# Kernel optimization log

Measured on AMD Instinct MI355X. Metric: run time of the kernel, lower is better.

## Reference

```python
import jax, jax.numpy as jnp
import numpy as np

OUT = 7          # roi_layer out_size
SR = 2           # roi_layer sample_num (sampling ratio)
STRIDES = (4, 8, 16, 32)
FINEST_SCALE = 56.0


def roi_align_level(feat, rois, spatial_scale):
    """RoIAlign (aligned=False, torchvision/mmdet classic) for all rois on one level.
    feat: (B, C, H, W), rois: (K, 5) [batch_idx, x1, y1, x2, y2] in image coords.
    Returns (K, C, OUT, OUT)."""
    B, C, H, W = feat.shape
    b = rois[:, 0].astype(jnp.int32)
    x1 = rois[:, 1] * spatial_scale
    y1 = rois[:, 2] * spatial_scale
    x2 = rois[:, 3] * spatial_scale
    y2 = rois[:, 4] * spatial_scale
    roi_w = jnp.maximum(x2 - x1, 1.0)
    roi_h = jnp.maximum(y2 - y1, 1.0)
    bin_w = roi_w / OUT
    bin_h = roi_h / OUT
    # per-bin sample offsets: (OUT, SR) fractional bin positions
    off = jnp.arange(OUT, dtype=jnp.float32)[:, None] + (jnp.arange(SR, dtype=jnp.float32)[None, :] + 0.5) / SR
    ys = y1[:, None, None] + off[None] * bin_h[:, None, None]   # (K, OUT, SR)
    xs = x1[:, None, None] + off[None] * bin_w[:, None, None]   # (K, OUT, SR)
    y = ys[:, :, :, None, None]                                  # (K, OUT, SR, 1, 1)
    x = xs[:, None, None, :, :]                                  # (K, 1, 1, OUT, SR)
    y, x = jnp.broadcast_arrays(y, x)                            # (K, OUT, SR, OUT, SR)
    valid = (y > -1.0) & (y < H) & (x > -1.0) & (x < W)
    yc = jnp.clip(y, 0.0, H - 1.0)
    xc = jnp.clip(x, 0.0, W - 1.0)
    y0 = jnp.floor(yc)
    x0 = jnp.floor(xc)
    ly = yc - y0
    lx = xc - x0
    hy = 1.0 - ly
    hx = 1.0 - lx
    y0i = y0.astype(jnp.int32)
    x0i = x0.astype(jnp.int32)
    y1i = jnp.minimum(y0i + 1, H - 1)
    x1i = jnp.minimum(x0i + 1, W - 1)
    bb = jnp.broadcast_to(b[:, None, None, None, None], y0i.shape)

    def g(yi, xi):
        # advanced indexing (batched gather) -> (K, OUT, SR, OUT, SR, C)
        return feat[bb, :, yi, xi]

    val = (hy * hx)[..., None] * g(y0i, x0i) \
        + (hy * lx)[..., None] * g(y0i, x1i) \
        + (ly * hx)[..., None] * g(y1i, x0i) \
        + (ly * lx)[..., None] * g(y1i, x1i)
    val = jnp.where(valid[..., None], val, 0.0)
    pooled = val.mean(axis=(2, 4))           # average SRxSR samples -> (K, OUT, OUT, C)
    return jnp.transpose(pooled, (0, 3, 1, 2))  # (K, C, OUT, OUT)


def map_roi_levels(rois, num_levels):
    scale = jnp.sqrt((rois[:, 3] - rois[:, 1] + 1.0) * (rois[:, 4] - rois[:, 2] + 1.0))
    lvl = jnp.floor(jnp.log2(scale / FINEST_SCALE + 1e-6))
    return jnp.clip(lvl, 0, num_levels - 1).astype(jnp.int32)


def setup_inputs() -> dict:
    key = jax.random.key(0)
    ks = jax.random.split(key, 10)
    B, C = 2, 256
    IMG_H, IMG_W = 800.0, 1344.0
    feats = {}
    shapes = [(B, C, 200, 336), (B, C, 100, 168), (B, C, 50, 84), (B, C, 25, 42)]
    for i, s in enumerate(shapes):
        feats[f"feat{i}"] = jax.random.normal(ks[i], s, dtype=jnp.float32)
    K = 1024
    bidx = jax.random.randint(ks[4], (K,), 0, B).astype(jnp.float32)
    # log-uniform box sizes in [16, ~724] px so all 4 FPN levels get rois
    w = 2.0 ** jax.random.uniform(ks[5], (K,), minval=4.0, maxval=9.5)
    h = 2.0 ** jax.random.uniform(ks[6], (K,), minval=4.0, maxval=9.5)
    cx = jax.random.uniform(ks[7], (K,), minval=0.0, maxval=IMG_W)
    cy = jax.random.uniform(ks[8], (K,), minval=0.0, maxval=IMG_H)
    x1 = jnp.clip(cx - w * 0.5, 0.0, IMG_W - 2.0)
    y1 = jnp.clip(cy - h * 0.5, 0.0, IMG_H - 2.0)
    x2 = jnp.clip(x1 + w, x1 + 1.0, IMG_W - 1.0)
    y2 = jnp.clip(y1 + h, y1 + 1.0, IMG_H - 1.0)
    rois = jnp.stack([bidx, x1, y1, x2, y2], axis=-1).astype(jnp.float32)
    feats["rois"] = rois
    return feats


def reference(feat0, feat1, feat2, feat3, rois):
    feats = [feat0, feat1, feat2, feat3]
    num_levels = len(feats)
    target_lvls = map_roi_levels(rois, num_levels)
    K = rois.shape[0]
    C = feats[0].shape[1]
    roi_feats = jnp.zeros((K, C, OUT, OUT), dtype=feats[0].dtype)
    for i in range(num_levels):
        ri = roi_align_level(feats[i], rois, 1.0 / STRIDES[i])
        mask = (target_lvls == i)[:, None, None, None]
        roi_feats = roi_feats + jnp.where(mask, ri, 0.0)
    return roi_feats
```

## Files before the change

### kernel.cpp

```cpp
#include <hip/hip_runtime.h>
#include <stdint.h>
#include <stddef.h>

#define C_TOTAL   256
#define CPG       4
#define NGROUPS   (C_TOTAL / CPG)
#define NBINS     49
#define NSAMP     196
#define TILE_D    1280
#define SD_STRIDE 16
#define BLOB_DW   (NSAMP * 8)
#define DESC_CHUNKS (BLOB_DW / 4)
#define WCHUNK    (DESC_CHUNKS / 4)

__global__ __launch_bounds__(256)
void roi_desc_kernel(const float* __restrict__ rois, int* __restrict__ ws_i,
                     int blobBase )
{
    const int k   = blockIdx.x;
    const int tid = threadIdx.x;

    const float bf  = rois[k * 5 + 0];
    const float rx1 = rois[k * 5 + 1];
    const float ry1 = rois[k * 5 + 2];
    const float rx2 = rois[k * 5 + 3];
    const float ry2 = rois[k * 5 + 4];
    const int   b   = (int)bf;

    const float scale = sqrtf((rx2 - rx1 + 1.0f) * (ry2 - ry1 + 1.0f));
    int lvl = (int)floorf(log2f(scale / 56.0f + 1e-6f));
    lvl = lvl < 0 ? 0 : (lvl > 3 ? 3 : lvl);

    int H, W;
    if      (lvl == 0) { H = 200; W = 336; }
    else if (lvl == 1) { H = 100; W = 168; }
    else if (lvl == 2) { H =  50; W =  84; }
    else               { H =  25; W =  42; }

    const float ss  = 1.0f / (float)(4 << lvl);
    const float x1s = rx1 * ss, y1s = ry1 * ss;
    const float x2s = rx2 * ss, y2s = ry2 * ss;
    const float roi_w = fmaxf(x2s - x1s, 1.0f);
    const float roi_h = fmaxf(y2s - y1s, 1.0f);
    const float bw = roi_w * (1.0f / 7.0f);
    const float bh = roi_h * (1.0f / 7.0f);

    const float Hm1 = (float)(H - 1), Wm1 = (float)(W - 1);
    const int ty0 = (int)floorf(fminf(fmaxf(y1s + 0.25f * bh, 0.0f), Hm1));
    const int tx0 = (int)floorf(fminf(fmaxf(x1s + 0.25f * bw, 0.0f), Wm1));
    const int ty1 = min((int)floorf(fminf(fmaxf(y1s + 6.75f * bh, 0.0f), Hm1)) + 1, H - 1);
    const int tx1 = min((int)floorf(fminf(fmaxf(x1s + 6.75f * bw, 0.0f), Wm1)) + 1, W - 1);
    const int fh = ty1 - ty0 + 1;
    const int fw = tx1 - tx0 + 1;

    int cpr = (fw + (tx0 & 3) + 3) >> 2;
    if (cpr > (W >> 2)) cpr = W >> 2;
    const bool use16 = (lvl < 3) && (fh * cpr <= TILE_D / 4);

    int rb, rowStride, chunks;
    if (use16) {
        rb = tx0 & ~3;
        if (rb + 4 * cpr > W) rb = W - 4 * cpr;
        rowStride = 4 * cpr;
        chunks = fh * cpr;
        if (chunks > TILE_D / 4) chunks = TILE_D / 4;
    } else {
        rb = tx0;
        rowStride = fw;
        chunks = fh * fw;
        if (chunks > TILE_D) chunks = TILE_D;
    }
    const uint32_t d = use16 ? (uint32_t)cpr : (uint32_t)fw;
    const uint32_t M = (1u << 22) / d + 1u;
    const int dW = W - rowStride;

    if (tid == 0) {
        int* sd = ws_i + k * SD_STRIDE;
        sd[0] = lvl;
        sd[1] = use16 ? 1 : 0;
        sd[2] = b * C_TOTAL * H * W + ty0 * W + rb;
        sd[3] = chunks;
        sd[4] = (int)M;
        sd[5] = dW;
        sd[6] = H * W;
    }

    if (tid < NSAMP) {
        const int iy = tid / 14;
        const int ix = tid - iy * 14;
        const float yy = y1s + ((float)iy * 0.5f + 0.25f) * bh;
        const float xx = x1s + ((float)ix * 0.5f + 0.25f) * bw;
        const bool valid = (yy > -1.0f) && (yy < (float)H) && (xx > -1.0f) && (xx < (float)W);
        const float yc  = fminf(fmaxf(yy, 0.0f), Hm1);
        const float xc  = fminf(fmaxf(xx, 0.0f), Wm1);
        const float y0f = floorf(yc);
        const float x0f = floorf(xc);
        const float ly = yc - y0f, lx = xc - x0f;
        const float hy = 1.0f - ly, hx = 1.0f - lx;
        const int y0  = (int)y0f, x0 = (int)x0f;
        const int y1i = min(y0 + 1, H - 1);
        const int x1i = min(x0 + 1, W - 1);
        const int r0 = (y0  - ty0) * rowStride - rb;
        const int r1 = (y1i - ty0) * rowStride - rb;
        const float v = valid ? 0.25f : 0.0f;
        float4* w4 = (float4*)(ws_i + blobBase + k * BLOB_DW);
        int4*   c4 = (int4*)  (ws_i + blobBase + k * BLOB_DW + 4 * NSAMP);
        w4[tid] = make_float4(hy * hx * v, hy * lx * v, ly * hx * v, ly * lx * v);
        c4[tid] = make_int4(r0 + x0, r0 + x1i, r1 + x0, r1 + x1i);
    }
}

__global__ __launch_bounds__(256, 6)
void roi_align_main(const float* __restrict__ f0,
                    const float* __restrict__ f1,
                    const float* __restrict__ f2,
                    const float* __restrict__ f3,
                    const int* __restrict__ ws_i,
                    float* __restrict__ out,
                    int blobBase)
{
    __shared__ __align__(16) float s_tile[CPG * TILE_D];
    __shared__ __align__(16) float s_desc[BLOB_DW];

    const int k    = blockIdx.y;
    const int g    = blockIdx.x;
    const int tid  = threadIdx.x;
    const int wv   = tid >> 6;
    const int lane = tid & 63;

    const int* sd = ws_i + k * SD_STRIDE;
    const int lvl     = sd[0];
    const int use16   = sd[1];
    const int srcBase = sd[2];
    const int chunks  = sd[3];
    const uint32_t M  = (uint32_t)sd[4];
    const int dW      = sd[5];
    const int HW      = sd[6];

    const float* feat = (lvl == 0) ? f0 : (lvl == 1) ? f1 : (lvl == 2) ? f2 : f3;

    {
        const int c = g * CPG + wv;
        const float* src = feat + srcBase + (size_t)c * (size_t)HW;
        float* dst = s_tile + wv * TILE_D;
        if (use16) {
            for (int start = 0; start < chunks; start += 64) {
                int s = (start + 64 > chunks) ? max(chunks - 64, 0) : start;
                int idx = s + lane;
                if (idx >= chunks) idx = chunks - 1;
                const int fy  = (int)(((uint32_t)idx * M) >> 22);
                const int off = (idx << 2) + fy * dW;
                __builtin_amdgcn_global_load_lds(
                    (const __attribute__((address_space(1))) uint32_t*)(src + off),
                    (__attribute__((address_space(3))) uint32_t*)(dst + (s << 2)),
                    16, 0, 0);
            }
        } else {
            for (int start = 0; start < chunks; start += 64) {
                int s = (start + 64 > chunks) ? max(chunks - 64, 0) : start;
                int idx = s + lane;
                if (idx >= chunks) idx = chunks - 1;
                const int fy  = (int)(((uint32_t)idx * M) >> 22);
                const int off = idx + fy * dW;
                __builtin_amdgcn_global_load_lds(
                    (const __attribute__((address_space(1))) uint32_t*)(src + off),
                    (__attribute__((address_space(3))) uint32_t*)(dst + s),
                    4, 0, 0);
            }
        }
    }

    {
        const float* bsrc = (const float*)(ws_i + blobBase + k * BLOB_DW);
        const int i0 = wv * WCHUNK;
        __builtin_amdgcn_global_load_lds(
            (const __attribute__((address_space(1))) uint32_t*)(bsrc + ((i0 + lane) << 2)),
            (__attribute__((address_space(3))) uint32_t*)(s_desc + (i0 << 2)),
            16, 0, 0);
        __builtin_amdgcn_global_load_lds(
            (const __attribute__((address_space(1))) uint32_t*)(bsrc + ((i0 + WCHUNK - 64 + lane) << 2)),
            (__attribute__((address_space(3))) uint32_t*)(s_desc + ((i0 + WCHUNK - 64) << 2)),
            16, 0, 0);
    }

    asm volatile("s_waitcnt vmcnt(0)" ::: "memory");
    __syncthreads();

    if (lane < NBINS) {
        const float*  t  = s_tile + wv * TILE_D;
        const float4* w4 = (const float4*)s_desc;
        const int4*   c4 = (const int4*)(s_desc + 4 * NSAMP);
        const int oy = lane / 7;
        const int ox = lane - oy * 7;
        const int sbase = oy * 28 + ox * 2;
        float acc = 0.0f;
#pragma unroll
        for (int sy = 0; sy < 2; ++sy) {
#pragma unroll
            for (int sx = 0; sx < 2; ++sx) {
                const int s = sbase + sy * 14 + sx;
                const float4 w  = w4[s];
                const int4   cc = c4[s];
                acc += w.x * t[cc.x] + w.y * t[cc.y]
                     + w.z * t[cc.z] + w.w * t[cc.w];
            }
        }
        const int c = g * CPG + wv;
        out[((size_t)k * C_TOTAL + c) * NBINS + lane] = acc;
    }
}

extern "C" void kernel_launch(void* const* d_in, const int* in_sizes, int n_in,
                              void* d_out, int out_size, void* d_ws, size_t ws_size,
                              hipStream_t stream) {
    const float* f0   = (const float*)d_in[0];
    const float* f1   = (const float*)d_in[1];
    const float* f2   = (const float*)d_in[2];
    const float* f3   = (const float*)d_in[3];
    const float* rois = (const float*)d_in[4];
    float* out = (float*)d_out;
    int*   ws  = (int*)d_ws;

    const int K = in_sizes[4] / 5;
    const int blobBase = K * SD_STRIDE;

    roi_desc_kernel<<<K, 256, 0, stream>>>(rois, ws, blobBase);

    dim3 grid(NGROUPS, K, 1);
    roi_align_main<<<grid, 256, 0, stream>>>(f0, f1, f2, f3, ws, out, blobBase);
}
```

Baseline: 146.1 us.

## Convert RoIAlign main kernel to persistent chains with double-buffered LDS prefetch

Replaces the one-block-per-(roi, channel-group) grid with a fixed grid of 8 chains per channel group. Each block loops over rois with stride 8 and double-buffers the feature tile and descriptor blob in LDS. The next roi's global-to-LDS loads are issued before computing the current one, and a counted vmcnt wait replaces the full drain. This is meant to hide load latency and cut per-block launch and setup overhead. In exchange, occupancy drops to 2 blocks per CU with twice the LDS per block, and total parallelism is much lower.

```diff
diff --git a/kernel.cpp b/kernel.cpp
--- a/kernel.cpp
+++ b/kernel.cpp
@@ -12,10 +12,11 @@
 #define BLOB_DW   (NSAMP * 8)
 #define DESC_CHUNKS (BLOB_DW / 4)
 #define WCHUNK    (DESC_CHUNKS / 4)
+#define NCHAIN    8
 
 __global__ __launch_bounds__(256)
 void roi_desc_kernel(const float* __restrict__ rois, int* __restrict__ ws_i,
-                     int blobBase )
+                     int blobBase)
 {
     const int k   = blockIdx.x;
     const int tid = threadIdx.x;
@@ -110,103 +111,146 @@
     }
 }
 
-__global__ __launch_bounds__(256, 6)
-void roi_align_main(const float* __restrict__ f0,
-                    const float* __restrict__ f1,
-                    const float* __restrict__ f2,
-                    const float* __restrict__ f3,
-                    const int* __restrict__ ws_i,
-                    float* __restrict__ out,
-                    int blobBase)
+struct SDesc { int lvl, use16, srcBase, chunks, M, dW, HW; };
+
+__device__ __forceinline__ SDesc load_sd(const int* __restrict__ p) {
+    SDesc s;
+    s.lvl = p[0]; s.use16 = p[1]; s.srcBase = p[2]; s.chunks = p[3];
+    s.M = p[4]; s.dW = p[5]; s.HW = p[6];
+    return s;
+}
+
+#define WV_CASE(N) case N: asm volatile("s_waitcnt vmcnt(" #N ")" ::: "memory"); break;
+__device__ __forceinline__ void wait_vm(int n) {
+    switch (n) {
+        WV_CASE(1) WV_CASE(2) WV_CASE(3) WV_CASE(4) WV_CASE(5)
+        WV_CASE(6) WV_CASE(7) WV_CASE(8) WV_CASE(9) WV_CASE(10)
+        WV_CASE(11) WV_CASE(12) WV_CASE(13) WV_CASE(14) WV_CASE(15)
+        WV_CASE(16) WV_CASE(17)
+        default: asm volatile("s_waitcnt vmcnt(0)" ::: "memory"); break;
+    }
+}
+
+__device__ __forceinline__ int stage_issue(float* __restrict__ tbuf, float* __restrict__ dbuf,
+                                           const SDesc& sd, int k, int g, int wv, int lane,
+                                           const float* __restrict__ f0, const float* __restrict__ f1,
+                                           const float* __restrict__ f2, const float* __restrict__ f3,
+                                           const int* __restrict__ ws_i, int blobBase)
 {
-    __shared__ __align__(16) float s_tile[CPG * TILE_D];
-    __shared__ __align__(16) float s_desc[BLOB_DW];
-
-    const int k    = blockIdx.y;
-    const int g    = blockIdx.x;
-    const int tid  = threadIdx.x;
-    const int wv   = tid >> 6;
-    const int lane = tid & 63;
-
-    const int* sd = ws_i + k * SD_STRIDE;
-    const int lvl     = sd[0];
-    const int use16   = sd[1];
-    const int srcBase = sd[2];
-    const int chunks  = sd[3];
-    const uint32_t M  = (uint32_t)sd[4];
-    const int dW      = sd[5];
-    const int HW      = sd[6];
-
-    const float* feat = (lvl == 0) ? f0 : (lvl == 1) ? f1 : (lvl == 2) ? f2 : f3;
-
-    {
-        const int c = g * CPG + wv;
-        const float* src = feat + srcBase + (size_t)c * (size_t)HW;
-        float* dst = s_tile + wv * TILE_D;
-        if (use16) {
-            for (int start = 0; start < chunks; start += 64) {
-                int s = (start + 64 > chunks) ? max(chunks - 64, 0) : start;
-                int idx = s + lane;
-                if (idx >= chunks) idx = chunks - 1;
-                const int fy  = (int)(((uint32_t)idx * M) >> 22);
-                const int off = (idx << 2) + fy * dW;
-                __builtin_amdgcn_global_load_lds(
-                    (const __attribute__((address_space(1))) uint32_t*)(src + off),
-                    (__attribute__((address_space(3))) uint32_t*)(dst + (s << 2)),
-                    16, 0, 0);
+    const float* feat = (sd.lvl == 0) ? f0 : (sd.lvl == 1) ? f1 : (sd.lvl == 2) ? f2 : f3;
+    const int c = g * CPG + wv;
+    const float* src = feat + sd.srcBase + (size_t)c * (size_t)sd.HW;
+    float* dst = tbuf + wv * TILE_D;
+    const uint32_t M = (uint32_t)sd.M;
+    const int chunks = sd.chunks, dW = sd.dW;
+    int n = 0;
+    if (sd.use16) {
+        for (int start = 0; start < chunks; start += 64) {
+            int s = (start + 64 > chunks) ? max(chunks - 64, 0) : start;
+            int idx = s + lane;
+            if (idx >= chunks) idx = chunks - 1;
+            const int fy  = (int)(((uint32_t)idx * M) >> 22);
+            const int off = (idx << 2) + fy * dW;
+            __builtin_amdgcn_global_load_lds(
+                (const __attribute__((address_space(1))) uint32_t*)(src + off),
+                (__attribute__((address_space(3))) uint32_t*)(dst + (s << 2)),
+                16, 0, 0);
+            ++n;
+        }
+    } else {
+        for (int start = 0; start < chunks; start += 64) {
+            int s = (start + 64 > chunks) ? max(chunks - 64, 0) : start;
+            int idx = s + lane;
+            if (idx >= chunks) idx = chunks - 1;
+            const int fy  = (int)(((uint32_t)idx * M) >> 22);
+            const int off = idx + fy * dW;
+            __builtin_amdgcn_global_load_lds(
+                (const __attribute__((address_space(1))) uint32_t*)(src + off),
+                (__attribute__((address_space(3))) uint32_t*)(dst + s),
+                4, 0, 0);
+            ++n;
+        }
+    }
+    const float* bsrc = (const float*)(ws_i + blobBase + k * BLOB_DW);
+    const int i0 = wv * WCHUNK;
+    __builtin_amdgcn_global_load_lds(
+        (const __attribute__((address_space(1))) uint32_t*)(bsrc + ((i0 + lane) << 2)),
+        (__attribute__((address_space(3))) uint32_t*)(dbuf + (i0 << 2)),
+        16, 0, 0);
+    __builtin_amdgcn_global_load_lds(
+        (const __attribute__((address_space(1))) uint32_t*)(bsrc + ((i0 + WCHUNK - 64 + lane) << 2)),
+        (__attribute__((address_space(3))) uint32_t*)(dbuf + ((i0 + WCHUNK - 64) << 2)),
+        16, 0, 0);
+    return n + 2;
+}
+
+__global__ __launch_bounds__(256, 2)
+void roi_align_chain(const float* __restrict__ f0,
+                     const float* __restrict__ f1,
+                     const float* __restrict__ f2,
+                     const float* __restrict__ f3,
+                     const int* __restrict__ ws_i,
+                     float* __restrict__ out,
+                     int blobBase, int K)
+{
+    __shared__ __align__(16) float s_tile[2][CPG * TILE_D];
+    __shared__ __align__(16) float s_desc[2][BLOB_DW];
+
+    const int g     = blockIdx.x;
+    const int chain = blockIdx.y;
+    const int tid   = threadIdx.x;
+    const int wv    = tid >> 6;
+    const int lane  = tid & 63;
+
+    if (chain >= K) return;
+
+    const int RPC = (K - chain + NCHAIN - 1) / NCHAIN;
+
+    SDesc sd0 = load_sd(ws_i + chain * SD_STRIDE);
+    stage_issue(s_tile[0], s_desc[0], sd0, chain, g, wv, lane, f0, f1, f2, f3, ws_i, blobBase);
+    int k1 = chain + NCHAIN; if (k1 >= K) k1 = K - 1;
+    SDesc sdn = load_sd(ws_i + k1 * SD_STRIDE);
+
+    for (int i = 0; i < RPC; ++i) {
+        const int k   = chain + i * NCHAIN;
+        const int cur = i & 1;
+
+        int nn = 0;
+        if (i + 1 < RPC)
+            nn = stage_issue(s_tile[cur ^ 1], s_desc[cur ^ 1], sdn, k + NCHAIN,
+                             g, wv, lane, f0, f1, f2, f3, ws_i, blobBase);
+
+        int kpre = chain + (i + 2) * NCHAIN;
+        if (kpre >= K) kpre = K - 1;
+        SDesc pre = load_sd(ws_i + kpre * SD_STRIDE);
+
+        wait_vm(nn);
+        __syncthreads();
+
+        if (lane < NBINS) {
+            const float*  t  = s_tile[cur] + wv * TILE_D;
+            const float4* w4 = (const float4*)s_desc[cur];
+            const int4*   c4 = (const int4*)(s_desc[cur] + 4 * NSAMP);
+            const int oy = lane / 7;
+            const int ox = lane - oy * 7;
+            const int sbase = oy * 28 + ox * 2;
+            float acc = 0.0f;
+#pragma unroll
+            for (int sy = 0; sy < 2; ++sy) {
+#pragma unroll
+                for (int sx = 0; sx < 2; ++sx) {
+                    const int s = sbase + sy * 14 + sx;
+                    const float4 w  = w4[s];
+                    const int4   cc = c4[s];
+                    acc += w.x * t[cc.x] + w.y * t[cc.y]
+                         + w.z * t[cc.z] + w.w * t[cc.w];
+                }
             }
-        } else {
-            for (int start = 0; start < chunks; start += 64) {
-                int s = (start + 64 > chunks) ? max(chunks - 64, 0) : start;
-                int idx = s + lane;
-                if (idx >= chunks) idx = chunks - 1;
-                const int fy  = (int)(((uint32_t)idx * M) >> 22);
-                const int off = idx + fy * dW;
-                __builtin_amdgcn_global_load_lds(
-                    (const __attribute__((address_space(1))) uint32_t*)(src + off),
-                    (__attribute__((address_space(3))) uint32_t*)(dst + s),
-                    4, 0, 0);
-            }
+            const int c = g * CPG + wv;
+            out[((size_t)k * C_TOTAL + c) * NBINS + lane] = acc;
         }
-    }
-
-    {
-        const float* bsrc = (const float*)(ws_i + blobBase + k * BLOB_DW);
-        const int i0 = wv * WCHUNK;
-        __builtin_amdgcn_global_load_lds(
-            (const __attribute__((address_space(1))) uint32_t*)(bsrc + ((i0 + lane) << 2)),
-            (__attribute__((address_space(3))) uint32_t*)(s_desc + (i0 << 2)),
-            16, 0, 0);
-        __builtin_amdgcn_global_load_lds(
-            (const __attribute__((address_space(1))) uint32_t*)(bsrc + ((i0 + WCHUNK - 64 + lane) << 2)),
-            (__attribute__((address_space(3))) uint32_t*)(s_desc + ((i0 + WCHUNK - 64) << 2)),
-            16, 0, 0);
-    }
-
-    asm volatile("s_waitcnt vmcnt(0)" ::: "memory");
-    __syncthreads();
-
-    if (lane < NBINS) {
-        const float*  t  = s_tile + wv * TILE_D;
-        const float4* w4 = (const float4*)s_desc;
-        const int4*   c4 = (const int4*)(s_desc + 4 * NSAMP);
-        const int oy = lane / 7;
-        const int ox = lane - oy * 7;
-        const int sbase = oy * 28 + ox * 2;
-        float acc = 0.0f;
-#pragma unroll
-        for (int sy = 0; sy < 2; ++sy) {
-#pragma unroll
-            for (int sx = 0; sx < 2; ++sx) {
-                const int s = sbase + sy * 14 + sx;
-                const float4 w  = w4[s];
-                const int4   cc = c4[s];
-                acc += w.x * t[cc.x] + w.y * t[cc.y]
-                     + w.z * t[cc.z] + w.w * t[cc.w];
-            }
-        }
-        const int c = g * CPG + wv;
-        out[((size_t)k * C_TOTAL + c) * NBINS + lane] = acc;
+        __syncthreads();
+        sdn = pre;
     }
 }
 
@@ -226,6 +270,6 @@
 
     roi_desc_kernel<<<K, 256, 0, stream>>>(rois, ws, blobBase);
 
-    dim3 grid(NGROUPS, K, 1);
-    roi_align_main<<<grid, 256, 0, stream>>>(f0, f1, f2, f3, ws, out, blobBase);
-}
+    dim3 grid(NGROUPS, NCHAIN, 1);
+    roi_align_chain<<<grid, 256, 0, stream>>>(f0, f1, f2, f3, ws, out, blobBase, K);
+}
```

Measured after the change: 197.3 us. +35.0%, slower.

## Sort RoIs by level and Morton-ordered center to improve L2 locality

Applied to the files above, without the earlier changes.

Adds a single-block bitonic sort kernel that orders RoIs by FPN level and a Z-order code of their box center, then launches the main kernel in that sorted order so neighbouring blocks read overlapping feature regions. The main kernel no longer stages the sample descriptor blob through LDS and instead reads weights and indices directly from global memory into registers; the smaller LDS footprint allows the occupancy hint to be raised from 6 to 7. The cost is an extra serial one-block launch plus a permuted descriptor copy. The sort path is only taken when K is at most 1024.

```diff
diff --git a/kernel.cpp b/kernel.cpp
--- a/kernel.cpp
+++ b/kernel.cpp
@@ -10,12 +10,12 @@
 #define TILE_D    1280
 #define SD_STRIDE 16
 #define BLOB_DW   (NSAMP * 8)
-#define DESC_CHUNKS (BLOB_DW / 4)
-#define WCHUNK    (DESC_CHUNKS / 4)
+#define SORTN     1024
+
 
 __global__ __launch_bounds__(256)
 void roi_desc_kernel(const float* __restrict__ rois, int* __restrict__ ws_i,
-                     int blobBase )
+                     int blobBase, int kbase)
 {
     const int k   = blockIdx.x;
     const int tid = threadIdx.x;
@@ -83,6 +83,19 @@
         sd[4] = (int)M;
         sd[5] = dW;
         sd[6] = H * W;
+        sd[7] = k;
+        const float cx = 0.5f * (rx1 + rx2);
+        const float cy = 0.5f * (ry1 + ry2);
+        int qx = (int)(cx * (64.0f / 1344.0f));
+        int qy = (int)(cy * (64.0f / 800.0f));
+        qx = qx < 0 ? 0 : (qx > 63 ? 63 : qx);
+        qy = qy < 0 ? 0 : (qy > 63 ? 63 : qy);
+        unsigned m = 0;
+#pragma unroll
+        for (int j = 0; j < 6; ++j)
+            m |= (((unsigned)(qx >> j) & 1u) << (2 * j)) |
+                 (((unsigned)(qy >> j) & 1u) << (2 * j + 1));
+        ws_i[kbase + k] = (int)(((unsigned)lvl << 22) | (m << 10) | (unsigned)k);
     }
 
     if (tid < NSAMP) {
@@ -103,32 +116,63 @@
         const int r0 = (y0  - ty0) * rowStride - rb;
         const int r1 = (y1i - ty0) * rowStride - rb;
         const float v = valid ? 0.25f : 0.0f;
-        float4* w4 = (float4*)(ws_i + blobBase + k * BLOB_DW);
-        int4*   c4 = (int4*)  (ws_i + blobBase + k * BLOB_DW + 4 * NSAMP);
+        float4* w4 = (float4*)(ws_i + blobBase + (size_t)k * BLOB_DW);
+        int4*   c4 = (int4*)  (ws_i + blobBase + (size_t)k * BLOB_DW + 4 * NSAMP);
         w4[tid] = make_float4(hy * hx * v, hy * lx * v, ly * hx * v, ly * lx * v);
         c4[tid] = make_int4(r0 + x0, r0 + x1i, r1 + x0, r1 + x1i);
     }
 }
 
-__global__ __launch_bounds__(256, 6)
+__global__ __launch_bounds__(256)
+void roi_sort_kernel(int* __restrict__ ws_i, int K, int kbase, int sbase)
+{
+    __shared__ unsigned skey[SORTN];
+    const int tid = threadIdx.x;
+
+    const bool do_sort = (K <= SORTN);
+    if (do_sort) {
+        for (int i = tid; i < SORTN; i += 256)
+            skey[i] = (i < K) ? (unsigned)ws_i[kbase + i] : 0xFFFFFFFFu;
+        __syncthreads();
+        for (unsigned size = 2; size <= SORTN; size <<= 1) {
+            for (unsigned stride = size >> 1; stride; stride >>= 1) {
+                for (int i = tid; i < SORTN; i += 256) {
+                    const unsigned p = (unsigned)i ^ stride;
+                    if (p > (unsigned)i) {
+                        const bool up = ((i & size) == 0);
+                        const unsigned a = skey[i], b = skey[p];
+                        if ((a > b) == up) { skey[i] = b; skey[p] = a; }
+                    }
+                }
+                __syncthreads();
+            }
+        }
+    }
+    for (int i = tid; i < K * SD_STRIDE; i += 256) {
+        const int rank = i >> 4, j = i & 15;
+        const int k = do_sort ? (int)(skey[rank] & 1023u) : rank;
+        ws_i[sbase + i] = ws_i[k * SD_STRIDE + j];
+    }
+}
+
+__global__ __launch_bounds__(256, 7)
 void roi_align_main(const float* __restrict__ f0,
                     const float* __restrict__ f1,
                     const float* __restrict__ f2,
                     const float* __restrict__ f3,
                     const int* __restrict__ ws_i,
                     float* __restrict__ out,
-                    int blobBase)
+                    int blobBase, int sbase)
 {
     __shared__ __align__(16) float s_tile[CPG * TILE_D];
-    __shared__ __align__(16) float s_desc[BLOB_DW];
-
-    const int k    = blockIdx.y;
+
+    const int rank = blockIdx.y;
     const int g    = blockIdx.x;
     const int tid  = threadIdx.x;
     const int wv   = tid >> 6;
     const int lane = tid & 63;
 
-    const int* sd = ws_i + k * SD_STRIDE;
+    const int* sd = ws_i + sbase + rank * SD_STRIDE;
     const int lvl     = sd[0];
     const int use16   = sd[1];
     const int srcBase = sd[2];
@@ -136,6 +180,7 @@
     const uint32_t M  = (uint32_t)sd[4];
     const int dW      = sd[5];
     const int HW      = sd[6];
+    const int k       = sd[7];
 
     const float* feat = (lvl == 0) ? f0 : (lvl == 1) ? f1 : (lvl == 2) ? f2 : f3;
 
@@ -170,40 +215,32 @@
         }
     }
 
-    {
-        const float* bsrc = (const float*)(ws_i + blobBase + k * BLOB_DW);
-        const int i0 = wv * WCHUNK;
-        __builtin_amdgcn_global_load_lds(
-            (const __attribute__((address_space(1))) uint32_t*)(bsrc + ((i0 + lane) << 2)),
-            (__attribute__((address_space(3))) uint32_t*)(s_desc + (i0 << 2)),
-            16, 0, 0);
-        __builtin_amdgcn_global_load_lds(
-            (const __attribute__((address_space(1))) uint32_t*)(bsrc + ((i0 + WCHUNK - 64 + lane) << 2)),
-            (__attribute__((address_space(3))) uint32_t*)(s_desc + ((i0 + WCHUNK - 64) << 2)),
-            16, 0, 0);
-    }
-
     asm volatile("s_waitcnt vmcnt(0)" ::: "memory");
     __syncthreads();
 
     if (lane < NBINS) {
         const float*  t  = s_tile + wv * TILE_D;
-        const float4* w4 = (const float4*)s_desc;
-        const int4*   c4 = (const int4*)(s_desc + 4 * NSAMP);
+        const float4* w4 = (const float4*)(ws_i + blobBase + (size_t)k * BLOB_DW);
+        const int4*   c4 = (const int4*)(ws_i + blobBase + (size_t)k * BLOB_DW + 4 * NSAMP);
         const int oy = lane / 7;
         const int ox = lane - oy * 7;
-        const int sbase = oy * 28 + ox * 2;
+        const int sbin = oy * 28 + ox * 2;
+
+        float4 w[4]; int4 cc[4];
+#pragma unroll
+        for (int sy = 0; sy < 2; ++sy)
+#pragma unroll
+            for (int sx = 0; sx < 2; ++sx) {
+                const int s = sbin + sy * 14 + sx;
+                w[sy * 2 + sx]  = w4[s];
+                cc[sy * 2 + sx] = c4[s];
+            }
+
         float acc = 0.0f;
 #pragma unroll
-        for (int sy = 0; sy < 2; ++sy) {
-#pragma unroll
-            for (int sx = 0; sx < 2; ++sx) {
-                const int s = sbase + sy * 14 + sx;
-                const float4 w  = w4[s];
-                const int4   cc = c4[s];
-                acc += w.x * t[cc.x] + w.y * t[cc.y]
-                     + w.z * t[cc.z] + w.w * t[cc.w];
-            }
+        for (int i = 0; i < 4; ++i) {
+            acc += w[i].x * t[cc[i].x] + w[i].y * t[cc[i].y]
+                 + w[i].z * t[cc[i].z] + w[i].w * t[cc[i].w];
         }
         const int c = g * CPG + wv;
         out[((size_t)k * C_TOTAL + c) * NBINS + lane] = acc;
@@ -223,9 +260,12 @@
 
     const int K = in_sizes[4] / 5;
     const int blobBase = K * SD_STRIDE;
-
-    roi_desc_kernel<<<K, 256, 0, stream>>>(rois, ws, blobBase);
+    const int kbase    = blobBase + K * BLOB_DW;
+    const int sbase    = kbase + SORTN;
+
+    roi_desc_kernel<<<K, 256, 0, stream>>>(rois, ws, blobBase, kbase);
+    roi_sort_kernel<<<1, 256, 0, stream>>>(ws, K, kbase, sbase);
 
     dim3 grid(NGROUPS, K, 1);
-    roi_align_main<<<grid, 256, 0, stream>>>(f0, f1, f2, f3, ws, out, blobBase);
-}
+    roi_align_main<<<grid, 256, 0, stream>>>(f0, f1, f2, f3, ws, out, blobBase, sbase);
+}
```

Result: slower. 179.2 us (+22.7%).
